# Kernel optimization log

Measured on AMD Instinct MI355X. Metric: run time of the kernel, lower is better.

Reference implementation:

```python
import jax, jax.numpy as jnp
import numpy as np

N, D = 65536, 64          # number of latent vectors, embedding dim
C, K = 4, 1024            # num_codebooks, num_embeddings
NOISE_STD = 1e-3          # torch Normal(0, noise_var) uses this as std (scale)
EPS_NORM = 1e-12
EPS_LOG = 1e-10


def setup_inputs() -> dict:
    key = jax.random.key(0)
    k1, k2, k3 = jax.random.split(key, 3)
    z = jax.random.normal(k1, (N, D), dtype=jnp.float32)
    # uniform_init: rand * (1/num_embeddings)
    codebook = jax.random.uniform(k2, (C, K, D), dtype=jnp.float32) * (1.0 / K)
    noise = jax.random.normal(k3, (N, D), dtype=jnp.float32)
    return {"z": z, "codebook": codebook, "noise": noise}


def _nearest(rem, cb):
    # squared euclidean distances [N, K]: ||r||^2 - 2 r.c + ||c||^2
    d2 = (jnp.sum(rem * rem, axis=1, keepdims=True)
          - 2.0 * (rem @ cb.T)
          + jnp.sum(cb * cb, axis=1))
    idx = jnp.argmin(d2, axis=1)          # [N] int
    q = cb[idx]                           # [N, D] gather of selected codewords
    return q, idx


def reference(z, codebook, noise):
    # Residual hard quantization across C codebooks (SF-DiVeQ steady-state branch)
    def step(rem, cb):
        q, idx = _nearest(rem, cb)
        return rem - q, (q, idx)

    _, (qs, idxs) = jax.lax.scan(step, z, codebook)  # qs: [C,N,D], idxs: [C,N]
    z_hard = jnp.sum(qs, axis=0)                     # [N, D]

    direction = z_hard - z
    rv = NOISE_STD * noise + direction
    normed = rv / jnp.clip(jnp.linalg.norm(rv, axis=1, keepdims=True), EPS_NORM)
    err_mag = jnp.linalg.norm(z_hard - z, axis=1, keepdims=True)
    z_q = z + err_mag * jax.lax.stop_gradient(normed)

    # perplexity per codebook: exp(-sum p log p), p = usage frequency
    counts = jax.vmap(lambda i: jnp.bincount(i, length=K))(idxs)  # [C, K]
    p = counts.astype(jnp.float32) / jnp.float32(N)
    perplexity = jnp.exp(-jnp.sum(p * jnp.log(p + EPS_LOG), axis=1))  # [C]

    return z_q, idxs, perplexity
```

## Files before the change

kernel.cpp:

```cpp
#include <hip/hip_runtime.h>
#include <math.h>


#define N_PTS 65536
#define DIM 64
#define NCB 4
#define KCB 1024
#define WAVES 4
#define KPART (KCB / WAVES)
#define ROWS_PER_BLK 64

typedef float f32x64 __attribute__((ext_vector_type(64)));
typedef float f32x8  __attribute__((ext_vector_type(8)));

__global__ __launch_bounds__(256) void prep_kernel(const float* __restrict__ cb,
    float* __restrict__ cnp, int* __restrict__ counts)
{
#pragma clang fp contract(off)
    int t = blockIdx.x * 256 + threadIdx.x;
    const float* row = cb + (size_t)t * DIM;
    float pr[8];
#pragma unroll
    for (int j = 0; j < 8; ++j) { float v = row[j]; pr[j] = v * v; }
#pragma unroll
    for (int i = 8; i < DIM; i += 8)
#pragma unroll
        for (int j = 0; j < 8; ++j) { float v = row[i + j]; pr[j] += v * v; }
    cnp[t] = ((pr[0] + pr[1]) + (pr[2] + pr[3])) + ((pr[4] + pr[5]) + (pr[6] + pr[7]));
    counts[t] = 0;
}

__global__ __launch_bounds__(256, 4) void rvq_kernel(
    const float* __restrict__ z, const float* __restrict__ cbook,
    const float* __restrict__ cnp, int* __restrict__ idxA)
{
#pragma clang fp contract(off)
    __shared__ float lm[WAVES][ROWS_PER_BLK];
    __shared__ int   li[WAVES][ROWS_PER_BLK];

    int lane = threadIdx.x & 63;
    int w = __builtin_amdgcn_readfirstlane(threadIdx.x >> 6);
    int n = blockIdx.x * ROWS_PER_BLK + lane;
    int kbase = w * KPART;

    f32x64 rz = *(const f32x64*)(z + (size_t)n * DIM);

    for (int c = 0; c < NCB; ++c) {
        f32x8 pr;
#pragma unroll
        for (int j = 0; j < 8; ++j) pr[j] = rz[j] * rz[j];
#pragma unroll
        for (int i = 8; i < DIM; i += 8)
#pragma unroll
            for (int j = 0; j < 8; ++j) pr[j] += rz[i + j] * rz[i + j];
        float srr = ((pr[0] + pr[1]) + (pr[2] + pr[3])) + ((pr[4] + pr[5]) + (pr[6] + pr[7]));

        const float* cb = cbook + (size_t)c * KCB * DIM;
        const float* cn = cnp + c * KCB;

        float m1 = 3.4028235e38f; int ix = kbase;
        for (int kk = 0; kk < KPART; kk += 8) {
            int k0 = kbase + kk;
            f32x8 a = (f32x8)0.0f;
#pragma unroll
            for (int d = 0; d < DIM; ++d) {
#pragma unroll
                for (int j = 0; j < 8; ++j)
                    a[j] = fmaf(rz[d], cb[(size_t)(k0 + j) * DIM + d], a[j]);
            }
#pragma unroll
            for (int j = 0; j < 8; ++j) {
                float t1 = 2.0f * a[j];
                float t2 = srr - t1;
                float dd = t2 + cn[k0 + j];
                if (dd < m1) { m1 = dd; ix = k0 + j; }
            }
        }
        lm[w][lane] = m1; li[w][lane] = ix;
        __syncthreads();

        float bm = lm[0][lane]; int bx = li[0][lane];
#pragma unroll
        for (int s = 1; s < WAVES; ++s) {
            float v = lm[s][lane]; int xi = li[s][lane];
            if (v < bm) { bm = v; bx = xi; }
        }
        if (w == 0) idxA[c * N_PTS + n] = bx;

        f32x64 q = *(const f32x64*)(cb + (size_t)bx * DIM);
        rz = rz - q;
        __syncthreads();
    }
}

__global__ __launch_bounds__(256) void zq_kernel(
    const float* __restrict__ z, const float* __restrict__ noise,
    const float* __restrict__ cbase, const int* __restrict__ idxA,
    float* __restrict__ out)
{
    int lane = threadIdx.x & 63;
    int n = blockIdx.x * 4 + (threadIdx.x >> 6);
    size_t e = (size_t)n * DIM + lane;
    double zd = z[e];
    double rd = zd;
#pragma unroll
    for (int cc = 0; cc < NCB; ++cc) {
        int id = idxA[cc * N_PTS + n];
        rd -= (double)cbase[((size_t)cc * KCB + id) * DIM + lane];
    }
    double dir = -rd;
    double rv = fma(1e-3, (double)noise[e], dir);
    double srv = rv * rv, sdir = dir * dir;
#pragma unroll
    for (int off = 32; off >= 1; off >>= 1) {
        srv  += __shfl_xor(srv, off);
        sdir += __shfl_xor(sdir, off);
    }
    double em = sqrt(sdir);
    double nn = sqrt(srv); nn = nn > 1e-12 ? nn : 1e-12;
    out[e] = (float)(zd + em * rv / nn);
}

__global__ __launch_bounds__(256) void hist_kernel(
    const int* __restrict__ idxA, float* __restrict__ out_idx, int* __restrict__ counts)
{
    int t = blockIdx.x * 256 + threadIdx.x;
    int v = idxA[t];
    out_idx[t] = (float)v;
    atomicAdd(&counts[(t >> 16) * KCB + v], 1);
}

__global__ __launch_bounds__(1024) void perp_kernel(const int* __restrict__ counts,
                                                    float* __restrict__ out)
{
    __shared__ double red[16];
    int tid = threadIdx.x, lane = tid & 63, w = tid >> 6;
    for (int c = 0; c < NCB; ++c) {
        double p = (double)counts[c * KCB + tid] / (double)N_PTS;
        double v = p * log(p + 1e-10);
#pragma unroll
        for (int off = 32; off >= 1; off >>= 1) v += __shfl_xor(v, off);
        if (lane == 0) red[w] = v;
        __syncthreads();
        if (tid == 0) {
            double ssum = 0.0;
            for (int i = 0; i < 16; ++i) ssum += red[i];
            out[c] = (float)exp(-ssum);
        }
        __syncthreads();
    }
}

extern "C" void kernel_launch(void* const* d_in, const int* in_sizes, int n_in,
                              void* d_out, int out_size, void* d_ws, size_t ws_size,
                              hipStream_t stream)
{
    const float* z     = (const float*)d_in[0];
    const float* cbook = (const float*)d_in[1];
    const float* noise = (const float*)d_in[2];
    float* out = (float*)d_out;
    char* ws = (char*)d_ws;

    int*   idxA   = (int*)  (ws);
    float* cnp    = (float*)(ws + 1048576);
    int*   counts = (int*)  (ws + 1064960);

    prep_kernel<<<16, 256, 0, stream>>>(cbook, cnp, counts);
    rvq_kernel<<<N_PTS / ROWS_PER_BLK, 256, 0, stream>>>(z, cbook, cnp, idxA);
    zq_kernel<<<N_PTS / 4, 256, 0, stream>>>(z, noise, cbook, idxA, out);
    hist_kernel<<<NCB * N_PTS / 256, 256, 0, stream>>>(
        idxA, out + (size_t)N_PTS * DIM, counts);
    perp_kernel<<<1, 1024, 0, stream>>>(
        counts, out + (size_t)N_PTS * DIM + (size_t)NCB * N_PTS);
}
```

Baseline: 725.8 us.

## Keep residual vectors in shared memory transposed to cut registers and raise occupancy

The residual vector for each row moves out of 64 per-thread registers into a transposed shared-memory array. The four waves load and update it cooperatively, each handling 16 dimensions. Launch bounds rise from 4 to 8 blocks per CU, so more waves can be resident to hide the latency of the codebook loads. In exchange, every FMA step now needs an LDS read per dimension, and the residual update needs an extra barrier-protected shared-memory round trip.

```diff
diff --git a/kernel.cpp b/kernel.cpp
--- a/kernel.cpp
+++ b/kernel.cpp
@@ -8,10 +8,9 @@
 #define KCB 1024
 #define WAVES 4
 #define KPART (KCB / WAVES)
-#define ROWS_PER_BLK 64
+#define ROWS 64
 
-typedef float f32x64 __attribute__((ext_vector_type(64)));
-typedef float f32x8  __attribute__((ext_vector_type(8)));
+typedef float f32x8 __attribute__((ext_vector_type(8)));
 
 __global__ __launch_bounds__(256) void prep_kernel(const float* __restrict__ cb,
     float* __restrict__ cnp, int* __restrict__ counts)
@@ -30,29 +29,41 @@
     counts[t] = 0;
 }
 
-__global__ __launch_bounds__(256, 4) void rvq_kernel(
+__global__ __launch_bounds__(256, 8) void rvq_kernel(
     const float* __restrict__ z, const float* __restrict__ cbook,
     const float* __restrict__ cnp, int* __restrict__ idxA)
 {
 #pragma clang fp contract(off)
-    __shared__ float lm[WAVES][ROWS_PER_BLK];
-    __shared__ int   li[WAVES][ROWS_PER_BLK];
+    __shared__ float rzT[DIM][ROWS];
+    __shared__ float lm[WAVES][ROWS];
+    __shared__ int   li[WAVES][ROWS];
 
     int lane = threadIdx.x & 63;
     int w = __builtin_amdgcn_readfirstlane(threadIdx.x >> 6);
-    int n = blockIdx.x * ROWS_PER_BLK + lane;
+    int n = blockIdx.x * ROWS + lane;
     int kbase = w * KPART;
 
-    f32x64 rz = *(const f32x64*)(z + (size_t)n * DIM);
+    {
+        const float4* zr = (const float4*)(z + (size_t)n * DIM + w * 16);
+#pragma unroll
+        for (int j = 0; j < 4; ++j) {
+            float4 v = zr[j];
+            rzT[w * 16 + j * 4 + 0][lane] = v.x;
+            rzT[w * 16 + j * 4 + 1][lane] = v.y;
+            rzT[w * 16 + j * 4 + 2][lane] = v.z;
+            rzT[w * 16 + j * 4 + 3][lane] = v.w;
+        }
+    }
+    __syncthreads();
 
     for (int c = 0; c < NCB; ++c) {
         f32x8 pr;
 #pragma unroll
-        for (int j = 0; j < 8; ++j) pr[j] = rz[j] * rz[j];
+        for (int j = 0; j < 8; ++j) { float v = rzT[j][lane]; pr[j] = v * v; }
 #pragma unroll
         for (int i = 8; i < DIM; i += 8)
 #pragma unroll
-            for (int j = 0; j < 8; ++j) pr[j] += rz[i + j] * rz[i + j];
+            for (int j = 0; j < 8; ++j) { float v = rzT[i + j][lane]; pr[j] += v * v; }
         float srr = ((pr[0] + pr[1]) + (pr[2] + pr[3])) + ((pr[4] + pr[5]) + (pr[6] + pr[7]));
 
         const float* cb = cbook + (size_t)c * KCB * DIM;
@@ -61,12 +72,14 @@
         float m1 = 3.4028235e38f; int ix = kbase;
         for (int kk = 0; kk < KPART; kk += 8) {
             int k0 = kbase + kk;
+            const float* c0 = cb + (size_t)k0 * DIM;
             f32x8 a = (f32x8)0.0f;
 #pragma unroll
             for (int d = 0; d < DIM; ++d) {
+                float rzd = rzT[d][lane];
 #pragma unroll
                 for (int j = 0; j < 8; ++j)
-                    a[j] = fmaf(rz[d], cb[(size_t)(k0 + j) * DIM + d], a[j]);
+                    a[j] = fmaf(rzd, c0[j * DIM + d], a[j]);
             }
 #pragma unroll
             for (int j = 0; j < 8; ++j) {
@@ -87,8 +100,18 @@
         }
         if (w == 0) idxA[c * N_PTS + n] = bx;
 
-        f32x64 q = *(const f32x64*)(cb + (size_t)bx * DIM);
-        rz = rz - q;
+        {
+            const float4* q4 = (const float4*)(cb + (size_t)bx * DIM + w * 16);
+#pragma unroll
+            for (int j = 0; j < 4; ++j) {
+                float4 q = q4[j];
+                int d = w * 16 + j * 4;
+                rzT[d + 0][lane] = rzT[d + 0][lane] - q.x;
+                rzT[d + 1][lane] = rzT[d + 1][lane] - q.y;
+                rzT[d + 2][lane] = rzT[d + 2][lane] - q.z;
+                rzT[d + 3][lane] = rzT[d + 3][lane] - q.w;
+            }
+        }
         __syncthreads();
     }
 }
@@ -166,7 +189,7 @@
     int*   counts = (int*)  (ws + 1064960);
 
     prep_kernel<<<16, 256, 0, stream>>>(cbook, cnp, counts);
-    rvq_kernel<<<N_PTS / ROWS_PER_BLK, 256, 0, stream>>>(z, cbook, cnp, idxA);
+    rvq_kernel<<<N_PTS / ROWS, 256, 0, stream>>>(z, cbook, cnp, idxA);
     zq_kernel<<<N_PTS / 4, 256, 0, stream>>>(z, noise, cbook, idxA, out);
     hist_kernel<<<NCB * N_PTS / 256, 256, 0, stream>>>(
         idxA, out + (size_t)N_PTS * DIM, counts);
```

Result: slower. 2.160 ms (+197.5%).

## Split RVQ into per-codebook kernels with codewords held in registers

Applied to the files above, without the earlier changes.

Replaces the fused rvq kernel with a per-codebook sequence of three kernels. The first updates the residual and its squared norm. The second gives each lane one codeword kept in registers and streams rows as wave-uniform loads, reducing with a 64-bit packed (distance, index) min via shuffles. The third merges the 16 partial minima per row. The aim is to cut the per-lane reloading of codebook rows in the old design, at the cost of more launches, a residual round-trip through the output buffer and an 8 MB partial-min buffer. Packing the index into the low bits means ties go to the lowest index, matching argmin. Comparing raw float bits as unsigned is only correct when distances are non-negative.

```diff
diff --git a/kernel.cpp b/kernel.cpp
--- a/kernel.cpp
+++ b/kernel.cpp
@@ -6,12 +6,12 @@
 #define DIM 64
 #define NCB 4
 #define KCB 1024
-#define WAVES 4
-#define KPART (KCB / WAVES)
-#define ROWS_PER_BLK 64
-
-typedef float f32x64 __attribute__((ext_vector_type(64)));
-typedef float f32x8  __attribute__((ext_vector_type(8)));
+#define PARTS 4
+#define KP (KCB / PARTS)
+#define RB 512
+#define RPB (N_PTS / RB)
+
+typedef unsigned long long u64;
 
 __global__ __launch_bounds__(256) void prep_kernel(const float* __restrict__ cb,
     float* __restrict__ cnp, int* __restrict__ counts)
@@ -30,67 +30,93 @@
     counts[t] = 0;
 }
 
-__global__ __launch_bounds__(256, 4) void rvq_kernel(
-    const float* __restrict__ z, const float* __restrict__ cbook,
-    const float* __restrict__ cnp, int* __restrict__ idxA)
+__global__ __launch_bounds__(256) void uprr_kernel(
+    const float* __restrict__ src, const float* __restrict__ cbc,
+    const int* __restrict__ ixp, float* __restrict__ rem, float* __restrict__ srr)
 {
 #pragma clang fp contract(off)
-    __shared__ float lm[WAVES][ROWS_PER_BLK];
-    __shared__ int   li[WAVES][ROWS_PER_BLK];
-
     int lane = threadIdx.x & 63;
-    int w = __builtin_amdgcn_readfirstlane(threadIdx.x >> 6);
-    int n = blockIdx.x * ROWS_PER_BLK + lane;
-    int kbase = w * KPART;
-
-    f32x64 rz = *(const f32x64*)(z + (size_t)n * DIM);
-
-    for (int c = 0; c < NCB; ++c) {
-        f32x8 pr;
-#pragma unroll
-        for (int j = 0; j < 8; ++j) pr[j] = rz[j] * rz[j];
-#pragma unroll
-        for (int i = 8; i < DIM; i += 8)
-#pragma unroll
-            for (int j = 0; j < 8; ++j) pr[j] += rz[i + j] * rz[i + j];
-        float srr = ((pr[0] + pr[1]) + (pr[2] + pr[3])) + ((pr[4] + pr[5]) + (pr[6] + pr[7]));
-
-        const float* cb = cbook + (size_t)c * KCB * DIM;
-        const float* cn = cnp + c * KCB;
-
-        float m1 = 3.4028235e38f; int ix = kbase;
-        for (int kk = 0; kk < KPART; kk += 8) {
-            int k0 = kbase + kk;
-            f32x8 a = (f32x8)0.0f;
-#pragma unroll
-            for (int d = 0; d < DIM; ++d) {
-#pragma unroll
-                for (int j = 0; j < 8; ++j)
-                    a[j] = fmaf(rz[d], cb[(size_t)(k0 + j) * DIM + d], a[j]);
-            }
-#pragma unroll
-            for (int j = 0; j < 8; ++j) {
-                float t1 = 2.0f * a[j];
-                float t2 = srr - t1;
-                float dd = t2 + cn[k0 + j];
-                if (dd < m1) { m1 = dd; ix = k0 + j; }
-            }
+    int n = blockIdx.x * 4 + (threadIdx.x >> 6);
+    size_t e = (size_t)n * DIM + lane;
+    float r = src[e];
+    if (cbc) {
+        int ix = ixp[n];
+        r = r - cbc[(size_t)ix * DIM + lane];
+        rem[e] = r;
+    }
+    float sq = r * r;
+    float pr = sq;
+#pragma unroll
+    for (int i = 1; i < 8; ++i) pr += __shfl(sq, (lane & 7) + 8 * i);
+    pr += __shfl_xor(pr, 1);
+    pr += __shfl_xor(pr, 2);
+    pr += __shfl_xor(pr, 4);
+    if (lane == 0) srr[n] = pr;
+}
+
+#define FMA4(RA, QA) \
+    acc = fmaf(RA.x, QA.x, acc); acc = fmaf(RA.y, QA.y, acc); \
+    acc = fmaf(RA.z, QA.z, acc); acc = fmaf(RA.w, QA.w, acc);
+
+__global__ __launch_bounds__(256, 3) void dist_kernel(
+    const float* __restrict__ src, const float* __restrict__ cbc,
+    const float* __restrict__ cnc, const float* __restrict__ srr,
+    u64* __restrict__ pm)
+{
+#pragma clang fp contract(off)
+    int lane = threadIdx.x & 63;
+    int wv = threadIdx.x >> 6;
+    int part = blockIdx.x & 3;
+    int rb = blockIdx.x >> 2;
+    int k = part * KP + wv * 64 + lane;
+
+    const float4* cw = (const float4*)(cbc + (size_t)k * DIM);
+    float4 q0 = cw[0],  q1 = cw[1],  q2 = cw[2],  q3 = cw[3];
+    float4 q4 = cw[4],  q5 = cw[5],  q6 = cw[6],  q7 = cw[7];
+    float4 q8 = cw[8],  q9 = cw[9],  q10 = cw[10], q11 = cw[11];
+    float4 q12 = cw[12], q13 = cw[13], q14 = cw[14], q15 = cw[15];
+    float cn = cnc[k];
+    int s = part * 4 + wv;
+
+    for (int r = 0; r < RPB; ++r) {
+        int n = rb * RPB + r;
+        const float4* rr = (const float4*)(src + (size_t)n * DIM);
+        float sr = srr[n];
+        float acc = 0.0f;
+        float4 ra;
+        ra = rr[0];  FMA4(ra, q0);   ra = rr[1];  FMA4(ra, q1);
+        ra = rr[2];  FMA4(ra, q2);   ra = rr[3];  FMA4(ra, q3);
+        ra = rr[4];  FMA4(ra, q4);   ra = rr[5];  FMA4(ra, q5);
+        ra = rr[6];  FMA4(ra, q6);   ra = rr[7];  FMA4(ra, q7);
+        ra = rr[8];  FMA4(ra, q8);   ra = rr[9];  FMA4(ra, q9);
+        ra = rr[10]; FMA4(ra, q10);  ra = rr[11]; FMA4(ra, q11);
+        ra = rr[12]; FMA4(ra, q12);  ra = rr[13]; FMA4(ra, q13);
+        ra = rr[14]; FMA4(ra, q14);  ra = rr[15]; FMA4(ra, q15);
+
+        float t1 = 2.0f * acc;
+        float t2 = sr - t1;
+        float dd = t2 + cn;
+        u64 key = ((u64)__float_as_uint(dd) << 32) | (unsigned)k;
+#pragma unroll
+        for (int off = 1; off < 64; off <<= 1) {
+            u64 o = __shfl_xor(key, off);
+            if (o < key) key = o;
         }
-        lm[w][lane] = m1; li[w][lane] = ix;
-        __syncthreads();
-
-        float bm = lm[0][lane]; int bx = li[0][lane];
-#pragma unroll
-        for (int s = 1; s < WAVES; ++s) {
-            float v = lm[s][lane]; int xi = li[s][lane];
-            if (v < bm) { bm = v; bx = xi; }
-        }
-        if (w == 0) idxA[c * N_PTS + n] = bx;
-
-        f32x64 q = *(const f32x64*)(cb + (size_t)bx * DIM);
-        rz = rz - q;
-        __syncthreads();
-    }
+        if (lane == 0) pm[(size_t)s * N_PTS + n] = key;
+    }
+}
+
+__global__ __launch_bounds__(256) void merge_kernel(
+    const u64* __restrict__ pm, int* __restrict__ idx)
+{
+    int n = blockIdx.x * 256 + threadIdx.x;
+    u64 m = pm[n];
+#pragma unroll
+    for (int s = 1; s < 16; ++s) {
+        u64 v = pm[(size_t)s * N_PTS + n];
+        if (v < m) m = v;
+    }
+    idx[n] = (int)(unsigned)(m & 0xffffffffu);
 }
 
 __global__ __launch_bounds__(256) void zq_kernel(
@@ -161,12 +187,27 @@
     float* out = (float*)d_out;
     char* ws = (char*)d_ws;
 
-    int*   idxA   = (int*)  (ws);
-    float* cnp    = (float*)(ws + 1048576);
-    int*   counts = (int*)  (ws + 1064960);
+    float* rem = out;
+
+    u64*   pm     = (u64*)  (ws);
+    int*   idxA   = (int*)  (ws + 8388608);
+    float* cnp    = (float*)(ws + 9437184);
+    int*   counts = (int*)  (ws + 9453568);
+    float* srr    = (float*)(ws + 9469952);
 
     prep_kernel<<<16, 256, 0, stream>>>(cbook, cnp, counts);
-    rvq_kernel<<<N_PTS / ROWS_PER_BLK, 256, 0, stream>>>(z, cbook, cnp, idxA);
+
+    for (int c = 0; c < NCB; ++c) {
+        const float* cb_prev = (c == 0) ? nullptr : cbook + (size_t)(c - 1) * KCB * DIM;
+        const int*   ix_prev = (c == 0) ? nullptr : idxA + (size_t)(c - 1) * N_PTS;
+        const float* usrc    = (c <= 1) ? z : rem;
+        const float* dsrc    = (c == 0) ? z : rem;
+        uprr_kernel<<<N_PTS / 4, 256, 0, stream>>>(usrc, cb_prev, ix_prev, rem, srr);
+        dist_kernel<<<PARTS * RB, 256, 0, stream>>>(
+            dsrc, cbook + (size_t)c * KCB * DIM, cnp + c * KCB, srr, pm);
+        merge_kernel<<<N_PTS / 256, 256, 0, stream>>>(pm, idxA + (size_t)c * N_PTS);
+    }
+
     zq_kernel<<<N_PTS / 4, 256, 0, stream>>>(z, noise, cbook, idxA, out);
     hist_kernel<<<NCB * N_PTS / 256, 256, 0, stream>>>(
         idxA, out + (size_t)N_PTS * DIM, counts);
```

After: 1.002 ms. 1.38x slower.
